# Kernel optimization log

Measured on AMD Instinct MI355X. Metric: run time of the kernel, lower is better.

The kernel has to match this reference:

```python
import jax, jax.numpy as jnp
import numpy as np
from jax import lax

S, B = 2048, 2048          # seq_len, batch (seq-first layout like nn.LSTM)
IN, H, OUT, L = 2, 4, 1, 4  # from module defaults


def setup_inputs() -> dict:
    key = jax.random.key(0)
    ks = jax.random.split(key, 11)
    s = 0.5  # ~ PyTorch init scale 1/sqrt(H)
    return {
        "x": jax.random.normal(ks[0], (S, B, IN), jnp.float32),
        "W_ih0": jax.random.normal(ks[1], (4 * H, IN), jnp.float32) * s,
        "W_hh0": jax.random.normal(ks[2], (4 * H, H), jnp.float32) * s,
        "b_ih0": jax.random.normal(ks[3], (4 * H,), jnp.float32) * s,
        "b_hh0": jax.random.normal(ks[4], (4 * H,), jnp.float32) * s,
        "W_ihr": jax.random.normal(ks[5], (L - 1, 4 * H, H), jnp.float32) * s,
        "W_hhr": jax.random.normal(ks[6], (L - 1, 4 * H, H), jnp.float32) * s,
        "b_ihr": jax.random.normal(ks[7], (L - 1, 4 * H), jnp.float32) * s,
        "b_hhr": jax.random.normal(ks[8], (L - 1, 4 * H), jnp.float32) * s,
        "W_out": jax.random.normal(ks[9], (OUT, H), jnp.float32) * s,
        "b_out": jax.random.normal(ks[10], (OUT,), jnp.float32) * s,
    }


def _lstm_layer(x, Wih, Whh, b):
    # x: [S, B, D_in]; PyTorch gate order: i, f, g, o
    Bsz = x.shape[1]
    Hh = Whh.shape[1]
    # precompute input contribution for all timesteps (batched GEMM)
    xg = jnp.einsum('sbd,gd->sbg', x, Wih) + b  # [S, B, 4H]

    def step(carry, xgt):
        h, c = carry
        gates = xgt + h @ Whh.T  # [B, 4H]
        i, f, g, o = jnp.split(gates, 4, axis=-1)
        c = jax.nn.sigmoid(f) * c + jax.nn.sigmoid(i) * jnp.tanh(g)
        h = jax.nn.sigmoid(o) * jnp.tanh(c)
        return (h, c), h

    init = (jnp.zeros((Bsz, Hh), x.dtype), jnp.zeros((Bsz, Hh), x.dtype))
    _, ys = lax.scan(step, init, xg)
    return ys  # [S, B, H]


def reference(x, W_ih0, W_hh0, b_ih0, b_hh0, W_ihr, W_hhr, b_ihr, b_hhr, W_out, b_out):
    h = _lstm_layer(x, W_ih0, W_hh0, b_ih0 + b_hh0)
    for l in range(W_ihr.shape[0]):  # fixed small layer loop
        h = _lstm_layer(h, W_ihr[l], W_hhr[l], b_ihr[l] + b_hhr[l])
    # dropout: identity in eval mode (deterministic reference)
    y = jnp.einsum('sbh,oh->sbo', h, W_out) + b_out  # linear head, [S, B, 1]
    return y
```

## Files before the change

kernel.cpp:

```cpp
#include <hip/hip_runtime.h>

#define S_LEN 2048
#define B_SZ 2048

template <int CTRL>
__device__ __forceinline__ float dppmov(float v) {
  int r = __builtin_amdgcn_update_dpp(0, __builtin_bit_cast(int, v), CTRL, 0xF,
                                      0xF, true);
  return __builtin_bit_cast(float, r);
}

__device__ __forceinline__ float rlane(float v, int l) {
  return __builtin_bit_cast(
      float, __builtin_amdgcn_readlane(__builtin_bit_cast(int, v), l));
}

#define TICK(ST, XVX, XVY, TT)                                                 \
  do {                                                                         \
    float i0 = is_row0 ? (XVX) : hin[0];                                       \
    float i1 = is_row0 ? (XVY) : hin[1];                                       \
    float t2 = fmaf(wh[1], hv[1], wh[0] * hv[0]);                              \
    float t3 = fmaf(wh[3], hv[3], wh[2] * hv[2]);                              \
    float t0 = fmaf(wi[1], i1, fmaf(wi[0], i0, bias));                         \
    float t1 = fmaf(wi[3], hin[3], wi[2] * hin[2]);                            \
    float a = (t0 + t1) + (t2 + t3);                                           \
    float e = __builtin_amdgcn_exp2f(a);                                       \
    float r = __builtin_amdgcn_rcpf(1.0f + e);                                 \
    float g = fmaf(mm, r, dd);                                                 \
    float q = g * dppmov<0x4E>(g);                  \
    float pig = dppmov<0x00>(q);                                               \
    float gf = dppmov<0x55>(g);                                                \
    float go = dppmov<0xFF>(g);                                                \
    c = fmaf(gf, c, pig);                                                      \
    float te = __builtin_amdgcn_exp2f(c * KT);                                 \
    float tr = __builtin_amdgcn_rcpf(1.0f + te);                               \
    float hh = go * fmaf(2.0f, tr, -1.0f);                                     \
    hv[0] = hh;                                                                \
    hv[1] = dppmov<0x124>(hh);                                                 \
    hv[2] = dppmov<0x128>(hh);                                                 \
    hv[3] = dppmov<0x12C>(hh);                                                 \
    slotf[wr_off] = hh;         \
    __builtin_amdgcn_wave_barrier();                                           \
    float4 nh = slot4[rd_slot];                                                \
    hin[0] = nh.x;                                                             \
    hin[1] = nh.y;                                                             \
    hin[2] = nh.z;                                                             \
    hin[3] = nh.w;                                                             \
    if (ST) {                                                                  \
      float y = fmaf(                                                          \
          wo[0], hv[0],                                                        \
          fmaf(wo[1], hv[1], fmaf(wo[2], hv[2], fmaf(wo[3], hv[3], bo))));     \
      if (do_store) out[(TT)*B_SZ + bidx] = y;                                 \
    }                                                                          \
  } while (0)

__global__ void __launch_bounds__(64, 2)
    lstm_kernel(const float *__restrict__ x, const float *__restrict__ Wih0,
                const float *__restrict__ Whh0, const float *__restrict__ bih0,
                const float *__restrict__ bhh0, const float *__restrict__ Wihr,
                const float *__restrict__ Whhr, const float *__restrict__ bihr,
                const float *__restrict__ bhhr, const float *__restrict__ Wout,
                const float *__restrict__ bout, float *__restrict__ out) {
  __shared__ __align__(16) float slotf[80];
  float4 *slot4 = (float4 *)slotf;

  const int lane = threadIdx.x & 63;
  const int ty = lane & 3;
  const int j = (lane >> 2) & 3;
  const int row = lane >> 4;
  const int bidx = blockIdx.x;
  const int wrow = ty * 4 + j;
  const bool is_row0 = (row == 0);
  const bool do_store = (lane == 48);
  const int wr_off = (ty == 0) ? ((row << 2) | j) : (16 + lane);
  const int rd_slot = (row + 3) & 3;

  slotf[lane] = 0.0f;
  slotf[16 + lane] = 0.0f;
  __builtin_amdgcn_wave_barrier();

  float pr = dppmov<0x124>((float)j);
  const int s = (((int)pr) - j) & 3;
  int rix[4] = {j, (j + s) & 3, (j + 2) & 3, (j + 3 * s) & 3};

  const float L2E = 1.4426950408889634f;
  const float kk = (ty == 2) ? -2.0f * L2E : -L2E;
  const float mm = (ty == 2) ? 2.0f : 1.0f;
  const float dd = (ty == 2) ? -1.0f : 0.0f;
  const float KT = -2.8853900817779268f;

  float wi[4], wh[4], bias;
  if (row == 0) {
    wi[0] = kk * Wih0[wrow * 2 + 0];
    wi[1] = kk * Wih0[wrow * 2 + 1];
    wi[2] = 0.0f;
    wi[3] = 0.0f;
#pragma unroll
    for (int k = 0; k < 4; ++k) wh[k] = kk * Whh0[wrow * 4 + rix[k]];
    bias = kk * (bih0[wrow] + bhh0[wrow]);
  } else {
    const int l = row - 1;
#pragma unroll
    for (int k = 0; k < 4; ++k) {
      wi[k] = kk * Wihr[l * 64 + wrow * 4 + k];
      wh[k] = kk * Whhr[l * 64 + wrow * 4 + rix[k]];
    }
    bias = kk * (bihr[l * 16 + wrow] + bhhr[l * 16 + wrow]);
  }
  float wo[4];
#pragma unroll
  for (int k = 0; k < 4; ++k) wo[k] = Wout[rix[k]];
  const float bo = bout[0];

  float hv[4] = {0, 0, 0, 0};
  float hin[4] = {0, 0, 0, 0};
  float c = 0.0f;

  const float2 *__restrict__ px = (const float2 *)x;

  const int l8 = lane & 7;
  auto ldx = [&](int base) -> float2 {
    int t = base + l8;
    if (t > S_LEN - 1) t = S_LEN - 1;
    return px[t * B_SZ + bidx];
  };

  {
    float2 xv = px[0 * B_SZ + bidx];
    TICK(false, xv.x, xv.y, 0);
    if (row > 0) { c = 0; hv[0] = hv[1] = hv[2] = hv[3] = 0; }
    xv = px[1 * B_SZ + bidx];
    TICK(false, xv.x, xv.y, 0);
    if (row > 1) { c = 0; hv[0] = hv[1] = hv[2] = hv[3] = 0; }
    xv = px[2 * B_SZ + bidx];
    TICK(false, xv.x, xv.y, 0);
    if (row > 2) { c = 0; hv[0] = hv[1] = hv[2] = hv[3] = 0; }
  }

  float2 xa = ldx(3);
  float2 xb = ldx(11);

  for (int it = 0; it < 256; ++it) {
    float2 xn = ldx(19 + it * 8);
#pragma unroll
    for (int u = 0; u < 8; ++u) {
      const int tt = it * 8 + u;
      float xvx = rlane(xa.x, u);
      float xvy = rlane(xa.y, u);
      TICK(true, xvx, xvy, tt);
    }
    xa = xb;
    xb = xn;
  }
}

extern "C" void kernel_launch(void *const *d_in, const int *in_sizes, int n_in,
                              void *d_out, int out_size, void *d_ws,
                              size_t ws_size, hipStream_t stream) {
  (void)in_sizes;
  (void)n_in;
  (void)out_size;
  (void)d_ws;
  (void)ws_size;
  const float *x = (const float *)d_in[0];
  const float *Wih0 = (const float *)d_in[1];
  const float *Whh0 = (const float *)d_in[2];
  const float *bih0 = (const float *)d_in[3];
  const float *bhh0 = (const float *)d_in[4];
  const float *Wihr = (const float *)d_in[5];
  const float *Whhr = (const float *)d_in[6];
  const float *bihr = (const float *)d_in[7];
  const float *bhhr = (const float *)d_in[8];
  const float *Wout = (const float *)d_in[9];
  const float *bout = (const float *)d_in[10];
  lstm_kernel<<<dim3(B_SZ), dim3(64), 0, stream>>>(
      x, Wih0, Whh0, bih0, bhh0, Wihr, Whhr, bihr, bhhr, Wout, bout,
      (float *)d_out);
}
```

Before: 453.6 us.

## Double-buffer inter-layer hidden state in LDS to take LDS read off critical path

Switches the layer wavefront to a two-step skew with ping-pong LDS slots. The next tick's inter-layer input is read at the start of the current tick, so the LDS load latency overlaps with the gate arithmetic instead of following the write and wave barrier. This lengthens the pipeline warmup to six ticks, adds a second input register buffer and alternating write offsets, and introduces an extra term in the gate sum.

```diff
diff --git a/kernel.cpp b/kernel.cpp
--- a/kernel.cpp
+++ b/kernel.cpp
@@ -15,15 +15,18 @@
       float, __builtin_amdgcn_readlane(__builtin_bit_cast(int, v), l));
 }
 
-#define TICK(ST, XVX, XVY, TT)                                                 \
+#define TICK(P, ST, XVX, XVY, TT, HC, HN)                                      \
   do {                                                                         \
-    float i0 = is_row0 ? (XVX) : hin[0];                                       \
-    float i1 = is_row0 ? (XVY) : hin[1];                                       \
+             \
+    HN = slot4[((P) ^ 1) * 4 + rd_slot];                                       \
+             \
+             \
+    float t0 = fmaf(wx0, (XVX), fmaf(wx1, (XVY), bias));                       \
+    float t1 = fmaf(wiH[1], HC.y, wiH[0] * HC.x);                              \
+    float t4 = fmaf(wiH[3], HC.w, wiH[2] * HC.z);                              \
     float t2 = fmaf(wh[1], hv[1], wh[0] * hv[0]);                              \
     float t3 = fmaf(wh[3], hv[3], wh[2] * hv[2]);                              \
-    float t0 = fmaf(wi[1], i1, fmaf(wi[0], i0, bias));                         \
-    float t1 = fmaf(wi[3], hin[3], wi[2] * hin[2]);                            \
-    float a = (t0 + t1) + (t2 + t3);                                           \
+    float a = ((t0 + t1) + t4) + (t2 + t3);                                    \
     float e = __builtin_amdgcn_exp2f(a);                                       \
     float r = __builtin_amdgcn_rcpf(1.0f + e);                                 \
     float g = fmaf(mm, r, dd);                                                 \
@@ -39,18 +42,23 @@
     hv[1] = dppmov<0x124>(hh);                                                 \
     hv[2] = dppmov<0x128>(hh);                                                 \
     hv[3] = dppmov<0x12C>(hh);                                                 \
-    slotf[wr_off] = hh;         \
+                     \
+    slotf[(P) ? wrB : wrA] = hh;                                               \
     __builtin_amdgcn_wave_barrier();                                           \
-    float4 nh = slot4[rd_slot];                                                \
-    hin[0] = nh.x;                                                             \
-    hin[1] = nh.y;                                                             \
-    hin[2] = nh.z;                                                             \
-    hin[3] = nh.w;                                                             \
     if (ST) {                                                                  \
       float y = fmaf(                                                          \
           wo[0], hv[0],                                                        \
           fmaf(wo[1], hv[1], fmaf(wo[2], hv[2], fmaf(wo[3], hv[3], bo))));     \
       if (do_store) out[(TT)*B_SZ + bidx] = y;                                 \
+    }                                                                          \
+  } while (0)
+
+#define WTICK(P, TAU, XVX, XVY, HC, HN)                                        \
+  do {                                                                         \
+    TICK(P, false, XVX, XVY, 0, HC, HN);                                       \
+    if (2 * row > (TAU)) {                                                     \
+      c = 0;                                                                   \
+      hv[0] = hv[1] = hv[2] = hv[3] = 0;                                       \
     }                                                                          \
   } while (0)
 
@@ -61,7 +69,7 @@
                 const float *__restrict__ Whhr, const float *__restrict__ bihr,
                 const float *__restrict__ bhhr, const float *__restrict__ Wout,
                 const float *__restrict__ bout, float *__restrict__ out) {
-  __shared__ __align__(16) float slotf[80];
+  __shared__ __align__(16) float slotf[112];
   float4 *slot4 = (float4 *)slotf;
 
   const int lane = threadIdx.x & 63;
@@ -70,13 +78,13 @@
   const int row = lane >> 4;
   const int bidx = blockIdx.x;
   const int wrow = ty * 4 + j;
-  const bool is_row0 = (row == 0);
   const bool do_store = (lane == 48);
-  const int wr_off = (ty == 0) ? ((row << 2) | j) : (16 + lane);
+  const int wrA = (ty == 0) ? ((row << 2) | j) : (96 + (lane & 15));
+  const int wrB = (ty == 0) ? (16 + ((row << 2) | j)) : (96 + (lane & 15));
   const int rd_slot = (row + 3) & 3;
 
   slotf[lane] = 0.0f;
-  slotf[16 + lane] = 0.0f;
+  if (lane < 48) slotf[64 + lane] = 0.0f;
   __builtin_amdgcn_wave_barrier();
 
   float pr = dppmov<0x124>((float)j);
@@ -89,20 +97,21 @@
   const float dd = (ty == 2) ? -1.0f : 0.0f;
   const float KT = -2.8853900817779268f;
 
-  float wi[4], wh[4], bias;
+  float wx0, wx1, wiH[4], wh[4], bias;
   if (row == 0) {
-    wi[0] = kk * Wih0[wrow * 2 + 0];
-    wi[1] = kk * Wih0[wrow * 2 + 1];
-    wi[2] = 0.0f;
-    wi[3] = 0.0f;
+    wx0 = kk * Wih0[wrow * 2 + 0];
+    wx1 = kk * Wih0[wrow * 2 + 1];
+    wiH[0] = wiH[1] = wiH[2] = wiH[3] = 0.0f;
 #pragma unroll
     for (int k = 0; k < 4; ++k) wh[k] = kk * Whh0[wrow * 4 + rix[k]];
     bias = kk * (bih0[wrow] + bhh0[wrow]);
   } else {
     const int l = row - 1;
+    wx0 = 0.0f;
+    wx1 = 0.0f;
 #pragma unroll
     for (int k = 0; k < 4; ++k) {
-      wi[k] = kk * Wihr[l * 64 + wrow * 4 + k];
+      wiH[k] = kk * Wihr[l * 64 + wrow * 4 + k];
       wh[k] = kk * Whhr[l * 64 + wrow * 4 + rix[k]];
     }
     bias = kk * (bihr[l * 16 + wrow] + bhhr[l * 16 + wrow]);
@@ -113,7 +122,8 @@
   const float bo = bout[0];
 
   float hv[4] = {0, 0, 0, 0};
-  float hin[4] = {0, 0, 0, 0};
+  float4 hinA = {0, 0, 0, 0};
+  float4 hinB = {0, 0, 0, 0};
   float c = 0.0f;
 
   const float2 *__restrict__ px = (const float2 *)x;
@@ -127,27 +137,34 @@
 
   {
     float2 xv = px[0 * B_SZ + bidx];
-    TICK(false, xv.x, xv.y, 0);
-    if (row > 0) { c = 0; hv[0] = hv[1] = hv[2] = hv[3] = 0; }
+    WTICK(0, 0, xv.x, xv.y, hinA, hinB);
     xv = px[1 * B_SZ + bidx];
-    TICK(false, xv.x, xv.y, 0);
-    if (row > 1) { c = 0; hv[0] = hv[1] = hv[2] = hv[3] = 0; }
+    WTICK(1, 1, xv.x, xv.y, hinB, hinA);
     xv = px[2 * B_SZ + bidx];
-    TICK(false, xv.x, xv.y, 0);
-    if (row > 2) { c = 0; hv[0] = hv[1] = hv[2] = hv[3] = 0; }
+    WTICK(0, 2, xv.x, xv.y, hinA, hinB);
+    xv = px[3 * B_SZ + bidx];
+    WTICK(1, 3, xv.x, xv.y, hinB, hinA);
+    xv = px[4 * B_SZ + bidx];
+    WTICK(0, 4, xv.x, xv.y, hinA, hinB);
+    xv = px[5 * B_SZ + bidx];
+    WTICK(1, 5, xv.x, xv.y, hinB, hinA);
   }
 
-  float2 xa = ldx(3);
-  float2 xb = ldx(11);
+  float2 xa = ldx(6);
+  float2 xb = ldx(14);
 
   for (int it = 0; it < 256; ++it) {
-    float2 xn = ldx(19 + it * 8);
+    float2 xn = ldx(22 + it * 8);
 #pragma unroll
     for (int u = 0; u < 8; ++u) {
       const int tt = it * 8 + u;
       float xvx = rlane(xa.x, u);
       float xvy = rlane(xa.y, u);
-      TICK(true, xvx, xvy, tt);
+      if ((u & 1) == 0) {
+        TICK(0, true, xvx, xvy, tt, hinA, hinB);
+      } else {
+        TICK(1, true, xvx, xvy, tt, hinB, hinA);
+      }
     }
     xa = xb;
     xb = xn;
```

Measured after the change: 459.5 us. Within noise of the previous version (+1.3%).

## Map LSTM layers to separate waves with double-buffered LDS and block barriers

Applied to the files above, without the earlier changes.

Each block now holds 4 waves, one per layer, and each wave packs 4 batch elements (16 lanes each) instead of one wave handling all 4 layers for a single batch element. Hidden states pass between layer waves through a double-buffered LDS slot array, with __syncthreads after every timestep, and the input x is prefetched per step into a register queue by the layer-0 wave. The aim is denser lane use and less per-wave serial work, at the cost of a block-wide barrier on every step of the recurrence.

```diff
diff --git a/kernel.cpp b/kernel.cpp
--- a/kernel.cpp
+++ b/kernel.cpp
@@ -10,74 +10,33 @@
   return __builtin_bit_cast(float, r);
 }
 
-__device__ __forceinline__ float rlane(float v, int l) {
-  return __builtin_bit_cast(
-      float, __builtin_amdgcn_readlane(__builtin_bit_cast(int, v), l));
-}
-
-#define TICK(ST, XVX, XVY, TT)                                                 \
-  do {                                                                         \
-    float i0 = is_row0 ? (XVX) : hin[0];                                       \
-    float i1 = is_row0 ? (XVY) : hin[1];                                       \
-    float t2 = fmaf(wh[1], hv[1], wh[0] * hv[0]);                              \
-    float t3 = fmaf(wh[3], hv[3], wh[2] * hv[2]);                              \
-    float t0 = fmaf(wi[1], i1, fmaf(wi[0], i0, bias));                         \
-    float t1 = fmaf(wi[3], hin[3], wi[2] * hin[2]);                            \
-    float a = (t0 + t1) + (t2 + t3);                                           \
-    float e = __builtin_amdgcn_exp2f(a);                                       \
-    float r = __builtin_amdgcn_rcpf(1.0f + e);                                 \
-    float g = fmaf(mm, r, dd);                                                 \
-    float q = g * dppmov<0x4E>(g);                  \
-    float pig = dppmov<0x00>(q);                                               \
-    float gf = dppmov<0x55>(g);                                                \
-    float go = dppmov<0xFF>(g);                                                \
-    c = fmaf(gf, c, pig);                                                      \
-    float te = __builtin_amdgcn_exp2f(c * KT);                                 \
-    float tr = __builtin_amdgcn_rcpf(1.0f + te);                               \
-    float hh = go * fmaf(2.0f, tr, -1.0f);                                     \
-    hv[0] = hh;                                                                \
-    hv[1] = dppmov<0x124>(hh);                                                 \
-    hv[2] = dppmov<0x128>(hh);                                                 \
-    hv[3] = dppmov<0x12C>(hh);                                                 \
-    slotf[wr_off] = hh;         \
-    __builtin_amdgcn_wave_barrier();                                           \
-    float4 nh = slot4[rd_slot];                                                \
-    hin[0] = nh.x;                                                             \
-    hin[1] = nh.y;                                                             \
-    hin[2] = nh.z;                                                             \
-    hin[3] = nh.w;                                                             \
-    if (ST) {                                                                  \
-      float y = fmaf(                                                          \
-          wo[0], hv[0],                                                        \
-          fmaf(wo[1], hv[1], fmaf(wo[2], hv[2], fmaf(wo[3], hv[3], bo))));     \
-      if (do_store) out[(TT)*B_SZ + bidx] = y;                                 \
-    }                                                                          \
-  } while (0)
-
-__global__ void __launch_bounds__(64, 2)
+__global__ void __launch_bounds__(256, 2)
     lstm_kernel(const float *__restrict__ x, const float *__restrict__ Wih0,
                 const float *__restrict__ Whh0, const float *__restrict__ bih0,
                 const float *__restrict__ bhh0, const float *__restrict__ Wihr,
                 const float *__restrict__ Whhr, const float *__restrict__ bihr,
                 const float *__restrict__ bhhr, const float *__restrict__ Wout,
                 const float *__restrict__ bout, float *__restrict__ out) {
-  __shared__ __align__(16) float slotf[80];
+  __shared__ __align__(16) float slotf[192];
   float4 *slot4 = (float4 *)slotf;
 
-  const int lane = threadIdx.x & 63;
-  const int ty = lane & 3;
-  const int j = (lane >> 2) & 3;
-  const int row = lane >> 4;
-  const int bidx = blockIdx.x;
+  const int tid = threadIdx.x;
+  const int lane = tid & 63;
+  const int row = tid >> 6;
+  const int b = lane >> 4;
+  const int G = lane & 15;
+  const int ty = G & 3;
+  const int j = G >> 2;
+  const int bidx = blockIdx.x * 4 + b;
   const int wrow = ty * 4 + j;
-  const bool is_row0 = (row == 0);
-  const bool do_store = (lane == 48);
-  const int wr_off = (ty == 0) ? ((row << 2) | j) : (16 + lane);
-  const int rd_slot = (row + 3) & 3;
+  const int rl = (row + 3) & 3;
+  const int rdq = rl * 4 + b;
+  const int wbase = row * 16 + b * 4 + j;
+  const int wrA = (ty == 0) ? wbase : (128 + lane);
+  const int wrB = (ty == 0) ? (64 + wbase) : (128 + lane);
 
-  slotf[lane] = 0.0f;
-  slotf[16 + lane] = 0.0f;
-  __builtin_amdgcn_wave_barrier();
+  if (tid < 192) slotf[tid] = 0.0f;
+  __syncthreads();
 
   float pr = dppmov<0x124>((float)j);
   const int s = (((int)pr) - j) & 3;
@@ -89,12 +48,10 @@
   const float dd = (ty == 2) ? -1.0f : 0.0f;
   const float KT = -2.8853900817779268f;
 
-  float wi[4], wh[4], bias;
+  float wx0 = 0.f, wx1 = 0.f, wiH[4] = {0, 0, 0, 0}, wh[4], bias;
   if (row == 0) {
-    wi[0] = kk * Wih0[wrow * 2 + 0];
-    wi[1] = kk * Wih0[wrow * 2 + 1];
-    wi[2] = 0.0f;
-    wi[3] = 0.0f;
+    wx0 = kk * Wih0[wrow * 2 + 0];
+    wx1 = kk * Wih0[wrow * 2 + 1];
 #pragma unroll
     for (int k = 0; k < 4; ++k) wh[k] = kk * Whh0[wrow * 4 + rix[k]];
     bias = kk * (bih0[wrow] + bhh0[wrow]);
@@ -102,7 +59,7 @@
     const int l = row - 1;
 #pragma unroll
     for (int k = 0; k < 4; ++k) {
-      wi[k] = kk * Wihr[l * 64 + wrow * 4 + k];
+      wiH[k] = kk * Wihr[l * 64 + wrow * 4 + k];
       wh[k] = kk * Whhr[l * 64 + wrow * 4 + rix[k]];
     }
     bias = kk * (bihr[l * 16 + wrow] + bhhr[l * 16 + wrow]);
@@ -113,44 +70,89 @@
   const float bo = bout[0];
 
   float hv[4] = {0, 0, 0, 0};
-  float hin[4] = {0, 0, 0, 0};
+  float4 hinA = {0, 0, 0, 0};
+  float4 hinB = {0, 0, 0, 0};
   float c = 0.0f;
 
   const float2 *__restrict__ px = (const float2 *)x;
+  float *__restrict__ outp = out;
 
-  const int l8 = lane & 7;
-  auto ldx = [&](int base) -> float2 {
-    int t = base + l8;
-    if (t > S_LEN - 1) t = S_LEN - 1;
-    return px[t * B_SZ + bidx];
+  auto tick = [&](int P, bool st, float2 xv, int tt, float4 &hc, float4 &hn) {
+    float a;
+    if (row == 0) {
+      float t0 = fmaf(wx1, xv.y, fmaf(wx0, xv.x, bias));
+      float t2 = fmaf(wh[1], hv[1], wh[0] * hv[0]);
+      float t3 = fmaf(wh[3], hv[3], wh[2] * hv[2]);
+      a = t0 + (t2 + t3);
+    } else {
+      float t0 = fmaf(wiH[1], hc.y, fmaf(wiH[0], hc.x, bias));
+      float t1 = fmaf(wiH[3], hc.w, wiH[2] * hc.z);
+      float t2 = fmaf(wh[1], hv[1], wh[0] * hv[0]);
+      float t3 = fmaf(wh[3], hv[3], wh[2] * hv[2]);
+      a = (t0 + t1) + (t2 + t3);
+    }
+    float e = __builtin_amdgcn_exp2f(a);
+    float r = __builtin_amdgcn_rcpf(1.0f + e);
+    float g = fmaf(mm, r, dd);
+    float q = g * dppmov<0x4E>(g);
+    float pig = dppmov<0x00>(q);
+    float gf = dppmov<0x55>(g);
+    float go = dppmov<0xFF>(g);
+    c = fmaf(gf, c, pig);
+    float te = __builtin_amdgcn_exp2f(c * KT);
+    float tr = __builtin_amdgcn_rcpf(1.0f + te);
+    float hh = go * fmaf(2.0f, tr, -1.0f);
+    hv[0] = hh;
+    hv[1] = dppmov<0x124>(hh);
+    hv[2] = dppmov<0x128>(hh);
+    hv[3] = dppmov<0x12C>(hh);
+    slotf[P ? wrB : wrA] = hh;
+    __syncthreads();
+    hn = slot4[P * 16 + rdq];
+    if (st && row == 3) {
+      float y = fmaf(
+          wo[0], hv[0],
+          fmaf(wo[1], hv[1], fmaf(wo[2], hv[2], fmaf(wo[3], hv[3], bo))));
+      if (G == 0) outp[tt * B_SZ + bidx] = y;
+    }
   };
 
   {
-    float2 xv = px[0 * B_SZ + bidx];
-    TICK(false, xv.x, xv.y, 0);
+    float2 xv = {0.f, 0.f};
+    if (row == 0) xv = px[0 * B_SZ + bidx];
+    tick(0, false, xv, 0, hinA, hinB);
     if (row > 0) { c = 0; hv[0] = hv[1] = hv[2] = hv[3] = 0; }
-    xv = px[1 * B_SZ + bidx];
-    TICK(false, xv.x, xv.y, 0);
+    if (row == 0) xv = px[1 * B_SZ + bidx];
+    tick(1, false, xv, 0, hinB, hinA);
     if (row > 1) { c = 0; hv[0] = hv[1] = hv[2] = hv[3] = 0; }
-    xv = px[2 * B_SZ + bidx];
-    TICK(false, xv.x, xv.y, 0);
+    if (row == 0) xv = px[2 * B_SZ + bidx];
+    tick(0, false, xv, 0, hinA, hinB);
     if (row > 2) { c = 0; hv[0] = hv[1] = hv[2] = hv[3] = 0; }
   }
 
-  float2 xa = ldx(3);
-  float2 xb = ldx(11);
+  float2 xq[8];
+  if (row == 0) {
+#pragma unroll
+    for (int u = 0; u < 8; ++u) xq[u] = px[(3 + u) * B_SZ + bidx];
+  }
 
   for (int it = 0; it < 256; ++it) {
-    float2 xn = ldx(19 + it * 8);
 #pragma unroll
     for (int u = 0; u < 8; ++u) {
       const int tt = it * 8 + u;
-      float xvx = rlane(xa.x, u);
-      float xvy = rlane(xa.y, u);
-      TICK(true, xvx, xvy, tt);
+      float2 xv = {0.f, 0.f};
+      if (row == 0) {
+        xv = xq[u];
+        int t = tt + 11;
+        if (t > S_LEN - 1) t = S_LEN - 1;
+        xq[u] = px[t * B_SZ + bidx];
+      }
+      if ((u & 1) == 0) {
+        tick(1, true, xv, tt, hinB, hinA);
+      } else {
+        tick(0, true, xv, tt, hinA, hinB);
+      }
     }
-    xa = xb;
-    xb = xn;
   }
 }
 
@@ -173,7 +175,7 @@
   const float *bhhr = (const float *)d_in[8];
   const float *Wout = (const float *)d_in[9];
   const float *bout = (const float *)d_in[10];
-  lstm_kernel<<<dim3(B_SZ), dim3(64), 0, stream>>>(
+  lstm_kernel<<<dim3(B_SZ / 4), dim3(256), 0, stream>>>(
       x, Wih0, Whh0, bih0, bhh0, Wihr, Whhr, bihr, bhhr, Wout, bout,
       (float *)d_out);
 }
```

Measured after the change: 997.9 us. 2.2x slower.

## Stage x inputs through LDS ring and batch output stores per wave

Applied to the files above, without the earlier changes.

Replaces the per-step readlane broadcast of x with a 16-step double-buffered LDS ring: layer-0 lanes read their input from the same float4 LDS load used for inter-layer hidden state, advancing a read offset. The tanh scaling constant is folded into the forget/input gate coefficients, and the h computation is reformed as one fma. Output stores are batched every 8 steps, and blocks get staggered s_sleep starts to desynchronize memory traffic. This adds LDS footprint and offset bookkeeping, and relies on correct ring timing.

```diff
diff --git a/kernel.cpp b/kernel.cpp
--- a/kernel.cpp
+++ b/kernel.cpp
@@ -10,48 +10,67 @@
   return __builtin_bit_cast(float, r);
 }
 
-__device__ __forceinline__ float rlane(float v, int l) {
-  return __builtin_bit_cast(
-      float, __builtin_amdgcn_readlane(__builtin_bit_cast(int, v), l));
-}
-
-#define TICK(ST, XVX, XVY, TT)                                                 \
+
+#define TICK(YOUT)                                                             \
   do {                                                                         \
-    float i0 = is_row0 ? (XVX) : hin[0];                                       \
-    float i1 = is_row0 ? (XVY) : hin[1];                                       \
+    float t0 = fmaf(wi[1], hin.y, fmaf(wi[0], hin.x, bias));                   \
+    float t1 = fmaf(wi[3], hin.w, wi[2] * hin.z);                              \
     float t2 = fmaf(wh[1], hv[1], wh[0] * hv[0]);                              \
     float t3 = fmaf(wh[3], hv[3], wh[2] * hv[2]);                              \
+    float a = (t0 + t1) + (t2 + t3);                                           \
+    float e = __builtin_amdgcn_exp2f(a);                                       \
+    float r = __builtin_amdgcn_rcpf(1.0f + e);                                 \
+    float g = fmaf(mm, r, dd);       \
+    float q = g * dppmov<0x4E>(g);                        \
+    float pig = dppmov<0x00>(q);                                               \
+    float gf = dppmov<0x55>(g);                                                \
+    float go = dppmov<0xFF>(g);                                                \
+    cKT = fmaf(gf, cKT, pig);          \
+    float te = __builtin_amdgcn_exp2f(cKT);                                    \
+    float tr = __builtin_amdgcn_rcpf(1.0f + te);                               \
+    float go2 = go + go;                                                       \
+    float hh = fmaf(go2, tr, -go);                         \
+    hv[0] = hh;                                                                \
+    hv[1] = dppmov<0x124>(hh);                                                 \
+    hv[2] = dppmov<0x128>(hh);                                                 \
+    hv[3] = dppmov<0x12C>(hh);                                                 \
+    slotf[wr_off] = hh;             \
+    __builtin_amdgcn_wave_barrier();                                           \
+    hin = *(const float4 *)(slotf + rdoff);    \
+    rdoff += rstep;                                                            \
+    YOUT = fmaf(wo[0], hv[0],                                                  \
+                fmaf(wo[1], hv[1],                                             \
+                     fmaf(wo[2], hv[2], fmaf(wo[3], hv[3], bo))));             \
+  } while (0)
+
+#define WTICK(XVX, XVY)                                                        \
+  do {                                                                         \
+    float i0 = is_row0 ? (XVX) : hin.x;                                        \
+    float i1 = is_row0 ? (XVY) : hin.y;                                        \
     float t0 = fmaf(wi[1], i1, fmaf(wi[0], i0, bias));                         \
-    float t1 = fmaf(wi[3], hin[3], wi[2] * hin[2]);                            \
+    float t1 = fmaf(wi[3], hin.w, wi[2] * hin.z);                              \
+    float t2 = fmaf(wh[1], hv[1], wh[0] * hv[0]);                              \
+    float t3 = fmaf(wh[3], hv[3], wh[2] * hv[2]);                              \
     float a = (t0 + t1) + (t2 + t3);                                           \
     float e = __builtin_amdgcn_exp2f(a);                                       \
     float r = __builtin_amdgcn_rcpf(1.0f + e);                                 \
     float g = fmaf(mm, r, dd);                                                 \
-    float q = g * dppmov<0x4E>(g);                  \
+    float q = g * dppmov<0x4E>(g);                                             \
     float pig = dppmov<0x00>(q);                                               \
     float gf = dppmov<0x55>(g);                                                \
     float go = dppmov<0xFF>(g);                                                \
-    c = fmaf(gf, c, pig);                                                      \
-    float te = __builtin_amdgcn_exp2f(c * KT);                                 \
+    cKT = fmaf(gf, cKT, pig);                                                  \
+    float te = __builtin_amdgcn_exp2f(cKT);                                    \
     float tr = __builtin_amdgcn_rcpf(1.0f + te);                               \
-    float hh = go * fmaf(2.0f, tr, -1.0f);                                     \
+    float go2 = go + go;                                                       \
+    float hh = fmaf(go2, tr, -go);                                             \
     hv[0] = hh;                                                                \
     hv[1] = dppmov<0x124>(hh);                                                 \
     hv[2] = dppmov<0x128>(hh);                                                 \
     hv[3] = dppmov<0x12C>(hh);                                                 \
-    slotf[wr_off] = hh;         \
+    slotf[wr_off] = hh;                                                        \
     __builtin_amdgcn_wave_barrier();                                           \
-    float4 nh = slot4[rd_slot];                                                \
-    hin[0] = nh.x;                                                             \
-    hin[1] = nh.y;                                                             \
-    hin[2] = nh.z;                                                             \
-    hin[3] = nh.w;                                                             \
-    if (ST) {                                                                  \
-      float y = fmaf(                                                          \
-          wo[0], hv[0],                                                        \
-          fmaf(wo[1], hv[1], fmaf(wo[2], hv[2], fmaf(wo[3], hv[3], bo))));     \
-      if (do_store) out[(TT)*B_SZ + bidx] = y;                                 \
-    }                                                                          \
+    hin = *(const float4 *)(slotf + hoff);                                     \
   } while (0)
 
 __global__ void __launch_bounds__(64, 2)
@@ -61,22 +80,27 @@
                 const float *__restrict__ Whhr, const float *__restrict__ bihr,
                 const float *__restrict__ bhhr, const float *__restrict__ Wout,
                 const float *__restrict__ bout, float *__restrict__ out) {
-  __shared__ __align__(16) float slotf[80];
-  float4 *slot4 = (float4 *)slotf;
+  __shared__ __align__(16) float slotf[208];
 
   const int lane = threadIdx.x & 63;
   const int ty = lane & 3;
   const int j = (lane >> 2) & 3;
   const int row = lane >> 4;
+  const int l16 = lane & 15;
   const int bidx = blockIdx.x;
   const int wrow = ty * 4 + j;
   const bool is_row0 = (row == 0);
   const bool do_store = (lane == 48);
-  const int wr_off = (ty == 0) ? ((row << 2) | j) : (16 + lane);
-  const int rd_slot = (row + 3) & 3;
+  const int wr_off = (ty == 0) ? ((row << 2) | j) : (144 + lane);
+  const int hoff = ((row + 3) & 3) * 4;
+  const int rbase = is_row0 ? 16 : hoff;
+  const int rstep = is_row0 ? 4 : 0;
+  const int rbig = is_row0 ? 128 : 0;
 
   slotf[lane] = 0.0f;
-  slotf[16 + lane] = 0.0f;
+  slotf[64 + lane] = 0.0f;
+  slotf[128 + lane] = 0.0f;
+  if (lane < 16) slotf[192 + lane] = 0.0f;
   __builtin_amdgcn_wave_barrier();
 
   float pr = dppmov<0x124>((float)j);
@@ -84,10 +108,10 @@
   int rix[4] = {j, (j + s) & 3, (j + 2) & 3, (j + 3 * s) & 3};
 
   const float L2E = 1.4426950408889634f;
+  const float KT = -2.8853900817779268f;
   const float kk = (ty == 2) ? -2.0f * L2E : -L2E;
-  const float mm = (ty == 2) ? 2.0f : 1.0f;
+  const float mm = (ty == 2) ? 2.0f : ((ty == 0) ? KT : 1.0f);
   const float dd = (ty == 2) ? -1.0f : 0.0f;
-  const float KT = -2.8853900817779268f;
 
   float wi[4], wh[4], bias;
   if (row == 0) {
@@ -113,44 +137,68 @@
   const float bo = bout[0];
 
   float hv[4] = {0, 0, 0, 0};
-  float hin[4] = {0, 0, 0, 0};
-  float c = 0.0f;
+  float4 hin = {0, 0, 0, 0};
+  float cKT = 0.0f;
 
   const float2 *__restrict__ px = (const float2 *)x;
 
-  const int l8 = lane & 7;
-  auto ldx = [&](int base) -> float2 {
-    int t = base + l8;
+  auto ldx16 = [&](int base) -> float2 {
+    int t = base + l16;
     if (t > S_LEN - 1) t = S_LEN - 1;
     return px[t * B_SZ + bidx];
   };
 
   {
     float2 xv = px[0 * B_SZ + bidx];
-    TICK(false, xv.x, xv.y, 0);
-    if (row > 0) { c = 0; hv[0] = hv[1] = hv[2] = hv[3] = 0; }
+    WTICK(xv.x, xv.y);
+    if (row > 0) { cKT = 0; hv[0] = hv[1] = hv[2] = hv[3] = 0; }
     xv = px[1 * B_SZ + bidx];
-    TICK(false, xv.x, xv.y, 0);
-    if (row > 1) { c = 0; hv[0] = hv[1] = hv[2] = hv[3] = 0; }
+    WTICK(xv.x, xv.y);
+    if (row > 1) { cKT = 0; hv[0] = hv[1] = hv[2] = hv[3] = 0; }
     xv = px[2 * B_SZ + bidx];
-    TICK(false, xv.x, xv.y, 0);
-    if (row > 2) { c = 0; hv[0] = hv[1] = hv[2] = hv[3] = 0; }
-  }
-
-  float2 xa = ldx(3);
-  float2 xb = ldx(11);
-
-  for (int it = 0; it < 256; ++it) {
-    float2 xn = ldx(19 + it * 8);
-#pragma unroll
-    for (int u = 0; u < 8; ++u) {
-      const int tt = it * 8 + u;
-      float xvx = rlane(xa.x, u);
-      float xvy = rlane(xa.y, u);
-      TICK(true, xvx, xvy, tt);
+    WTICK(xv.x, xv.y);
+    if (row > 2) { cKT = 0; hv[0] = hv[1] = hv[2] = hv[3] = 0; }
+  }
+
+  {
+    float2 w0 = ldx16(3);
+    float2 w1 = ldx16(19);
+    *(float2 *)(slotf + 16 + 4 * l16) = w0;
+    *(float2 *)(slotf + 80 + 4 * l16) = w1;
+    __builtin_amdgcn_wave_barrier();
+  }
+  float2 gxa = ldx16(35);
+  float2 gxb = ldx16(51);
+
+  int rdoff = rbase;
+  hin = *(const float4 *)(slotf + rdoff);
+  rdoff += rstep;
+
+  if (blockIdx.x & 1024) __builtin_amdgcn_s_sleep(4);
+  if (blockIdx.x & 256) __builtin_amdgcn_s_sleep(2);
+  if (blockIdx.x & 4) __builtin_amdgcn_s_sleep(1);
+
+  float ya[8];
+  for (int k = 0; k < 64; ++k) {
+    const int tb = k * 32;
+#pragma unroll
+    for (int u = 0; u < 32; ++u) {
+      if (u == 15) {
+        *(float2 *)(slotf + 16 + 4 * l16) = gxa;
+        gxa = ldx16(67 + 32 * k);
+      }
+      if (u == 31) {
+        *(float2 *)(slotf + 80 + 4 * l16) = gxb;
+        gxb = ldx16(83 + 32 * k);
+        rdoff -= rbig;
+      }
+      TICK(ya[u & 7]);
+      if ((u & 7) == 7 && do_store) {
+#pragma unroll
+        for (int v = 0; v < 8; ++v)
+          out[(tb + (u & 24) + v) * B_SZ + bidx] = ya[v];
+      }
     }
-    xa = xb;
-    xb = xn;
   }
 }
 
```

Result: faster. 384.9 us (-15.1%).
